# Optimization experiments

Measured on AMD Instinct MI355X. Metric: run time of the kernel, lower is better.

Reference implementation:

```python
import jax, jax.numpy as jnp
import numpy as np

M0, M1 = 16, 8          # scalar / vector multiplicities (16x0e + 8x1o)
NB = 16                  # number_of_basis
RMAX = 8.0               # max_radius
N_NODES, N_EDGES = 10000, 160000
WNUM = M0*M0 + M0*M1 + M1*M1 + M1*M0  # 576, tp weight_numel


def sus(t):
    """e3nn soft_unit_step: exp(-1/t) for t>0 else 0."""
    safe = jnp.where(t > 0, t, 1.0)
    return jnp.where(t > 0, jnp.exp(-1.0 / safe), 0.0)


def setup_inputs():
    key = jax.random.key(0)
    ks = jax.random.split(key, 12)
    D = M0 + 3 * M1  # 40
    x = jax.random.normal(ks[0], (N_NODES, D), jnp.float32)
    edge_index = jax.random.randint(ks[1], (2, N_EDGES), 0, N_NODES, jnp.int32)
    edge_attr = jax.random.normal(ks[2], (N_EDGES, 4), jnp.float32)  # sh lmax=1
    node_attr = jnp.ones((N_NODES, 1), jnp.float32)
    batch = jnp.zeros((N_NODES,), jnp.int32)
    amf = jax.random.uniform(ks[3], (N_EDGES, 1), jnp.float32) * RMAX  # edge lengths
    Wq0 = jax.random.normal(ks[4], (M0, M0), jnp.float32)
    Wq1 = jax.random.normal(ks[5], (M1, M1), jnp.float32)
    Wk1 = jax.random.normal(ks[6], (NB, 16), jnp.float32)
    Wk2 = jax.random.normal(ks[7], (16, WNUM), jnp.float32)
    Wv1 = jax.random.normal(ks[8], (NB, 16), jnp.float32)
    Wv2 = jax.random.normal(ks[9], (16, WNUM), jnp.float32)
    Wd0 = jax.random.normal(ks[10], (M0, M0), jnp.float32)
    Wd1 = jax.random.normal(ks[11], (M1, M1), jnp.float32)
    return dict(x=x, edge_index=edge_index, edge_attr=edge_attr, node_attr=node_attr,
                batch=batch, additional_message_features=amf,
                Wq0=Wq0, Wq1=Wq1, Wk1=Wk1, Wk2=Wk2, Wv1=Wv1, Wv2=Wv2, Wd0=Wd0, Wd1=Wd1)


def reference(x, edge_index, edge_attr, node_attr, batch, additional_message_features,
              Wq0, Wq1, Wk1, Wk2, Wv1, Wv2, Wd0, Wd1):
    n = x.shape[0]
    src, dst = edge_index[0], edge_index[1]
    d = additional_message_features.reshape(-1)  # [E]

    # soft_one_hot_linspace(basis='smooth_finite', cutoff=True) * sqrt(NB)
    centers = jnp.linspace(0.0, RMAX, NB + 2)[1:-1]
    step = RMAX / (NB + 1)
    diff = (d[:, None] - centers) / step
    emb = (1.14136 * np.exp(2.0)) * sus(diff + 1.0) * sus(1.0 - diff) * np.sqrt(NB)  # [E,NB]
    cutoff = sus(10.0 * (1.0 - d / RMAX))  # [E]

    # split irreps: scalars [*,M0], vectors [*,M1,3]
    x0 = x[:, :M0]
    x1 = x[:, M0:].reshape(n, M1, 3)

    # q = Linear(input_irreps -> hidden_irreps): per-irrep linear, 1/sqrt(fan_in)
    q0 = (x0 @ Wq0) / np.sqrt(M0)
    q1 = jnp.einsum('nui,uw->nwi', x1, Wq1) / np.sqrt(M1)

    # radial MLPs producing per-edge tensor-product weights
    def radial(W1, W2):
        h = jax.nn.silu((emb @ W1) / np.sqrt(NB))
        return (h @ W2) / np.sqrt(16.0)  # [E, WNUM]
    wk = radial(Wk1, Wk2)
    wv = radial(Wv1, Wv2)

    xs0, xs1 = x0[src], x1[src]           # gather by edge source
    sh0, sh1 = edge_attr[:, 0], edge_attr[:, 1:4]
    dot11 = jnp.einsum('eui,ei->eu', xs1, sh1) / np.sqrt(3.0)  # 1o x 1o -> 0e CG

    def fctp(w):
        # FullyConnectedTensorProduct(input, sh, out) with per-edge weights.
        s1 = M0 * M0
        s2 = s1 + M0 * M1
        s3 = s2 + M1 * M1
        w1 = w[:, :s1].reshape(-1, M0, M0)   # 0e x 0e -> 0e
        w2 = w[:, s1:s2].reshape(-1, M0, M1) # 0e x 1o -> 1o
        w3 = w[:, s2:s3].reshape(-1, M1, M1) # 1o x 0e -> 1o
        w4 = w[:, s3:].reshape(-1, M1, M0)   # 1o x 1o -> 0e
        norm = 1.0 / np.sqrt(M0 + M1)        # path fan-in normalization
        o0 = (jnp.einsum('euw,eu->ew', w1, xs0 * sh0[:, None]) +
              jnp.einsum('euw,eu->ew', w4, dot11)) * norm            # [E,M0]
        o1 = (jnp.einsum('euw,eu,ei->ewi', w2, xs0, sh1) +
              jnp.einsum('euw,eui->ewi', w3, xs1 * sh0[:, None, None])) * norm  # [E,M1,3]
        return o0, o1

    k0, k1 = fctp(wk)
    v0, v1 = fctp(wv)

    # dot: FullyConnectedTensorProduct(hidden, hidden, '0e') with shared weights
    score = (jnp.einsum('eu,ev,uv->e', q0[dst], k0, Wd0) +
             jnp.einsum('eui,evi,uv->e', q1[dst], k1, Wd1) / np.sqrt(3.0)) / np.sqrt(M0*M0 + M1*M1)

    expv = cutoff * jnp.exp(score)                                   # [E]
    z = jax.ops.segment_sum(expv, dst, num_segments=n)               # [N]
    z = jnp.where(z == 0, 1.0, z)
    alpha = expv / z[dst]
    we = jnp.sqrt(jax.nn.relu(alpha))                                # alpha.relu().sqrt()
    v = jnp.concatenate([v0, v1.reshape(-1, 3 * M1)], axis=1)        # [E,40]
    return jax.ops.segment_sum(we[:, None] * v, dst, num_segments=n) # [N,40]
```

## Files before the change

kernel.cpp:

```cpp
#include <hip/hip_runtime.h>
#include <hip/hip_bf16.h>

#define E_CNT 160000
#define N_CNT 10000

#define INV_STEP   2.125f
#define EMB_C      33.734292f
#define INVS320    0.05590170f
#define INVS8      0.35355339f
#define INV_SQRT3  0.57735027f
#define KSCALE     0.051031036f

#define OFF_FLAG   0
#define OFF_EAF    400016
#define OFF_AMFF   1040016
#define OFF_WK1F   1200656
#define OFF_WV1F   1200912
#define OFF_P      1219600
#define OFF_EXPV   1619600
#define OFF_VBUF   1779600
#define OFF_DEG    8179600
#define OFF_Z      8179600
#define OFF_DEG2   8189600
#define OFF_START  8199600
#define OFF_START2 8209601
#define OFF_CURS   8219602
#define OFF_CURS2  8229602
#define OFF_DPOS   8239602
#define OFF_ELIST2 8399602
#define OFF_G      8559632


static __device__ __forceinline__ float bf2f(__hip_bfloat16 b) { return __bfloat162float(b); }
static __device__ __forceinline__ float sanitize(float v) {
    return fminf(fmaxf(v, -1e30f), 1e30f);
}
static __device__ __forceinline__ unsigned short f2bf(float f) {
    unsigned x = __float_as_uint(f);
    unsigned r = (x + 0x7fffu + ((x >> 16) & 1u)) >> 16;
    return (unsigned short)r;
}
static __device__ __forceinline__ float bflo(unsigned u) { return __uint_as_float(u << 16); }
static __device__ __forceinline__ float bfhi(unsigned u) { return __uint_as_float(u & 0xffff0000u); }
static __device__ __forceinline__ float2 bfp(unsigned u) {
    float2 r; r.x = bflo(u); r.y = bfhi(u); return r;
}

static __device__ __forceinline__ float4 load4(const void* p, int i4, int f32)
{
    if (f32) return ((const float4*)p)[i4];
    uint2 u = ((const uint2*)p)[i4];
    float4 r;
    r.x = bflo(u.x); r.y = bfhi(u.x);
    r.z = bflo(u.y); r.w = bfhi(u.y);
    return r;
}

static __device__ __forceinline__ void ld8(const float* p, float (&r)[8])
{
    float4 a = ((const float4*)p)[0];
    float4 b = ((const float4*)p)[1];
    r[0] = a.x; r[1] = a.y; r[2] = a.z; r[3] = a.w;
    r[4] = b.x; r[5] = b.y; r[6] = b.z; r[7] = b.w;
}
static __device__ __forceinline__ void ld8(const __hip_bfloat16* p, float (&r)[8])
{
    uint4 u = *(const uint4*)p;
    r[0] = bflo(u.x); r[1] = bfhi(u.x); r[2] = bflo(u.y); r[3] = bfhi(u.y);
    r[4] = bflo(u.z); r[5] = bfhi(u.z); r[6] = bflo(u.w); r[7] = bfhi(u.w);
}

__global__ __launch_bounds__(256) void init_kernel(
    const unsigned short* __restrict__ xb, float* __restrict__ ws)
{
    const int idx = blockIdx.x * 256 + threadIdx.x;
    if (idx < 20000) ((int*)(ws + OFF_DEG))[idx] = 0;
    if (blockIdx.x == 0 && threadIdx.x < 64) {
        const int lane = threadIdx.x;
        unsigned e0 = (unsigned)((xb[2 * lane] >> 7) & 0xFF);
        unsigned e1 = (unsigned)((xb[128 + 2 * lane] >> 7) & 0xFF);
        int c = (e0 >= 141 ? 1 : 0) + (e1 >= 141 ? 1 : 0);
#pragma unroll
        for (int off = 1; off < 64; off <<= 1) c += __shfl_xor(c, off);
        if (lane == 0) *(int*)ws = (c >= 8) ? 1 : 0;
    }
}

static __device__ __forceinline__ void do_prep(
    const void* __restrict__ ea, const void* __restrict__ amf,
    const void* __restrict__ Wk1, const void* __restrict__ Wv1,
    const int* __restrict__ ei, float* __restrict__ ws, int i, int f32)
{
    if (i < 160000) ((float4*)(ws + OFF_EAF))[i] = load4(ea, i, f32);
    if (i < 40000) {
        ((float4*)(ws + OFF_AMFF))[i] = load4(amf, i, f32);
#pragma unroll
        for (int k = 0; k < 4; ++k) {
            atomicAdd((int*)(ws + OFF_DEG)  + ei[E_CNT + 4 * i + k], 1);
            atomicAdd((int*)(ws + OFF_DEG2) + ei[4 * i + k], 1);
        }
    }
    if (i < 64) {
        ((float4*)(ws + OFF_WK1F))[i] = load4(Wk1, i, f32);
        ((float4*)(ws + OFF_WV1F))[i] = load4(Wv1, i, f32);
    }
}

template <typename T>
static __device__ __forceinline__ void build_G(
    const T* __restrict__ x, const T* __restrict__ W2b, int n, int p, int c, float* __restrict__ ws)
{
    float xs[40];
#pragma unroll
    for (int q = 0; q < 5; ++q) ld8(x + n * 40 + q * 8, *(float(*)[8])(xs + q * 8));
    const T* W2 = W2b + c * 576;

    float out[96];
#pragma unroll
    for (int k = 0; k < 96; ++k) out[k] = 0.f;

#pragma unroll
    for (int u = 0; u < 16; ++u) {
        float r0[8], r1[8];
        ld8(W2 + u * 16, r0);
        ld8(W2 + u * 16 + 8, r1);
        const float xv = xs[u];
#pragma unroll
        for (int w = 0; w < 8; ++w) {
            out[w]     = fmaf(r0[w], xv, out[w]);
            out[8 + w] = fmaf(r1[w], xv, out[8 + w]);
        }
    }
#pragma unroll
    for (int u = 0; u < 16; ++u) {
        float r[8];
        ld8(W2 + 256 + u * 8, r);
        const float xv = xs[u];
#pragma unroll
        for (int w = 0; w < 8; ++w) out[16 + w] = fmaf(r[w], xv, out[16 + w]);
    }
#pragma unroll
    for (int u = 0; u < 8; ++u) {
        float r[8];
        ld8(W2 + 384 + u * 8, r);
        const float a0 = xs[16 + u * 3 + 0];
        const float a1 = xs[16 + u * 3 + 1];
        const float a2 = xs[16 + u * 3 + 2];
#pragma unroll
        for (int w = 0; w < 8; ++w) {
            out[24 + w * 3 + 0] = fmaf(r[w], a0, out[24 + w * 3 + 0]);
            out[24 + w * 3 + 1] = fmaf(r[w], a1, out[24 + w * 3 + 1]);
            out[24 + w * 3 + 2] = fmaf(r[w], a2, out[24 + w * 3 + 2]);
        }
    }
#pragma unroll
    for (int u = 0; u < 8; ++u) {
        float r0[8], r1[8];
        ld8(W2 + 448 + u * 16, r0);
        ld8(W2 + 448 + u * 16 + 8, r1);
        const float a0 = xs[16 + u * 3 + 0];
        const float a1 = xs[16 + u * 3 + 1];
        const float a2 = xs[16 + u * 3 + 2];
#pragma unroll
        for (int w = 0; w < 8; ++w) {
            out[48 + w * 3 + 0] = fmaf(r0[w], a0, out[48 + w * 3 + 0]);
            out[48 + w * 3 + 1] = fmaf(r0[w], a1, out[48 + w * 3 + 1]);
            out[48 + w * 3 + 2] = fmaf(r0[w], a2, out[48 + w * 3 + 2]);
            out[48 + (8 + w) * 3 + 0] = fmaf(r1[w], a0, out[48 + (8 + w) * 3 + 0]);
            out[48 + (8 + w) * 3 + 1] = fmaf(r1[w], a1, out[48 + (8 + w) * 3 + 1]);
            out[48 + (8 + w) * 3 + 2] = fmaf(r1[w], a2, out[48 + (8 + w) * 3 + 2]);
        }
    }
#pragma unroll
    for (int k = 0; k < 48; ++k) out[48 + k] *= INV_SQRT3;

    uint4 ov[12];
    unsigned* ou = (unsigned*)ov;
#pragma unroll
    for (int k = 0; k < 48; ++k)
        ou[k] = (unsigned)f2bf(out[2 * k]) | ((unsigned)f2bf(out[2 * k + 1]) << 16);
    uint4* gb = (uint4*)(ws + OFF_G) + (size_t)(p * 16 + c) * 120000 + n;
#pragma unroll
    for (int q = 0; q < 12; ++q) gb[q * 10000] = ov[q];
}

template <typename T>
static __device__ __forceinline__ void build_P(
    const T* __restrict__ x, const T* __restrict__ Wq0, const T* __restrict__ Wq1,
    const T* __restrict__ Wd0, const T* __restrict__ Wd1, int n, float* __restrict__ ws)
{
    float xs[40];
#pragma unroll
    for (int q = 0; q < 5; ++q) ld8(x + n * 40 + q * 8, *(float(*)[8])(xs + q * 8));

    float q0[16];
#pragma unroll
    for (int w = 0; w < 16; ++w) q0[w] = 0.f;
#pragma unroll
    for (int u = 0; u < 16; ++u) {
        float r0[8], r1[8];
        ld8(Wq0 + u * 16, r0);
        ld8(Wq0 + u * 16 + 8, r1);
        const float xv = xs[u];
#pragma unroll
        for (int w = 0; w < 8; ++w) {
            q0[w]     = fmaf(r0[w], xv, q0[w]);
            q0[8 + w] = fmaf(r1[w], xv, q0[8 + w]);
        }
    }
#pragma unroll
    for (int w = 0; w < 16; ++w) q0[w] *= 0.25f;

    float p0[16];
#pragma unroll
    for (int v = 0; v < 16; ++v) p0[v] = 0.f;
#pragma unroll
    for (int w = 0; w < 16; ++w) {
        float r0[8], r1[8];
        ld8(Wd0 + w * 16, r0);
        ld8(Wd0 + w * 16 + 8, r1);
        const float qv = q0[w];
#pragma unroll
        for (int v = 0; v < 8; ++v) {
            p0[v]     = fmaf(r0[v], qv, p0[v]);
            p0[8 + v] = fmaf(r1[v], qv, p0[8 + v]);
        }
    }
    float* pn = ws + OFF_P + n * 40;
#pragma unroll
    for (int v = 0; v < 16; ++v) pn[v] = sanitize(p0[v] * INVS320);

    float q1[24];
#pragma unroll
    for (int k = 0; k < 24; ++k) q1[k] = 0.f;
#pragma unroll
    for (int u = 0; u < 8; ++u) {
        float r[8];
        ld8(Wq1 + u * 8, r);
        const float a0 = xs[16 + u * 3 + 0];
        const float a1 = xs[16 + u * 3 + 1];
        const float a2 = xs[16 + u * 3 + 2];
#pragma unroll
        for (int w = 0; w < 8; ++w) {
            q1[w * 3 + 0] = fmaf(r[w], a0, q1[w * 3 + 0]);
            q1[w * 3 + 1] = fmaf(r[w], a1, q1[w * 3 + 1]);
            q1[w * 3 + 2] = fmaf(r[w], a2, q1[w * 3 + 2]);
        }
    }
#pragma unroll
    for (int k = 0; k < 24; ++k) q1[k] *= INVS8;

    float p1[24];
#pragma unroll
    for (int k = 0; k < 24; ++k) p1[k] = 0.f;
#pragma unroll
    for (int w = 0; w < 8; ++w) {
        float r[8];
        ld8(Wd1 + w * 8, r);
        const float b0 = q1[w * 3 + 0];
        const float b1 = q1[w * 3 + 1];
        const float b2 = q1[w * 3 + 2];
#pragma unroll
        for (int v = 0; v < 8; ++v) {
            p1[v * 3 + 0] = fmaf(r[v], b0, p1[v * 3 + 0]);
            p1[v * 3 + 1] = fmaf(r[v], b1, p1[v * 3 + 1]);
            p1[v * 3 + 2] = fmaf(r[v], b2, p1[v * 3 + 2]);
        }
    }
    const float sc = INVS320 * INV_SQRT3;
#pragma unroll
    for (int k = 0; k < 24; ++k) pn[16 + k] = sanitize(p1[k] * sc);
}

__global__ __launch_bounds__(256) void gp_kernel(
    const void* __restrict__ x,
    const void* __restrict__ Wq0, const void* __restrict__ Wq1,
    const void* __restrict__ Wk2, const void* __restrict__ Wv2,
    const void* __restrict__ Wd0, const void* __restrict__ Wd1,
    const void* __restrict__ ea, const void* __restrict__ amf,
    const void* __restrict__ Wk1, const void* __restrict__ Wv1,
    const int* __restrict__ ei,
    float* __restrict__ ws)
{
    const int f32 = *(const int*)ws;
    const int tid = threadIdx.x;
    const int blk = blockIdx.x;
    if (blk < 625) {
        do_prep(ea, amf, Wk1, Wv1, ei, ws, blk * 256 + tid, f32);
        return;
    }
    if (blk < 1875) {
        const int t = (blk - 625) * 256 + tid;
        const int p   = t / 160000;
        const int rem = t - p * 160000;
        const int c   = rem / 10000;
        const int n   = rem - c * 10000;
        const void* W2b = p ? Wv2 : Wk2;
        if (f32) build_G((const float*)x, (const float*)W2b, n, p, c, ws);
        else     build_G((const __hip_bfloat16*)x, (const __hip_bfloat16*)W2b, n, p, c, ws);
        return;
    }
    {
        const int n = (blk - 1875) * 256 + tid;
        if (n >= N_CNT) return;
        if (f32) build_P((const float*)x, (const float*)Wq0, (const float*)Wq1,
                         (const float*)Wd0, (const float*)Wd1, n, ws);
        else     build_P((const __hip_bfloat16*)x, (const __hip_bfloat16*)Wq0,
                         (const __hip_bfloat16*)Wq1, (const __hip_bfloat16*)Wd0,
                         (const __hip_bfloat16*)Wd1, n, ws);
    }
}

__global__ __launch_bounds__(512) void scan_kernel(float* __restrict__ ws)
{
    __shared__ int ssum[512];
    const int t    = threadIdx.x;
    const int half = t >> 8;
    const int lt   = t & 255;
    int* deg   = (int*)(ws + (half ? OFF_DEG2   : OFF_DEG));
    int* start = (int*)(ws + (half ? OFF_START2 : OFF_START));
    int* curs  = (int*)(ws + (half ? OFF_CURS2  : OFF_CURS));
    const int base = lt * 40;
    int s = 0;
    for (int k = 0; k < 40; ++k) {
        int idx = base + k;
        if (idx < N_CNT) s += deg[idx];
    }
    ssum[t] = s;
    __syncthreads();
    for (int off = 1; off < 256; off <<= 1) {
        int v = (lt >= off) ? ssum[t - off] : 0;
        __syncthreads();
        ssum[t] += v;
        __syncthreads();
    }
    int run = ssum[t] - s;
    for (int k = 0; k < 40; ++k) {
        int idx = base + k;
        if (idx < N_CNT) {
            start[idx] = run;
            curs[idx]  = run;
            run += deg[idx];
        }
    }
    if (lt == 255) start[N_CNT] = E_CNT;
    __syncthreads();
    for (int k = t; k < N_CNT; k += 512) ws[OFF_Z + k] = 0.f;
}

__global__ __launch_bounds__(256) void fill_kernel(const int* __restrict__ ei, float* __restrict__ ws)
{
    const int e = blockIdx.x * 256 + threadIdx.x;
    int pd = atomicAdd((int*)(ws + OFF_CURS)  + ei[E_CNT + e], 1);
    int ps = atomicAdd((int*)(ws + OFF_CURS2) + ei[e], 1);
    ((int*)(ws + OFF_ELIST2))[ps] = e;
    ((int*)(ws + OFF_DPOS))[ps]   = pd;
}

static __device__ __forceinline__ void load48p(unsigned (&ub)[48], const uint4* __restrict__ p0)
{
#pragma unroll
    for (int q = 0; q < 12; ++q) {
        uint4 v = p0[(size_t)q * 10000];
        ub[4 * q + 0] = v.x; ub[4 * q + 1] = v.y;
        ub[4 * q + 2] = v.z; ub[4 * q + 3] = v.w;
    }
}

static __device__ __forceinline__ void accum48(const unsigned (&ub)[48], float hc, float sh0,
    float s1x, float s1y, float s1z,
    float (&o0)[16], float (&o1)[24], float (&t2a)[8])
{
    const float hs = hc * sh0;
#define GVAL(k) (((k) & 1) ? bfhi(ub[(k) >> 1]) : bflo(ub[(k) >> 1]))
#pragma unroll
    for (int w = 0; w < 16; ++w) o0[w] = fmaf(hs, GVAL(w), o0[w]);
#pragma unroll
    for (int w = 0; w < 8; ++w) t2a[w] = fmaf(hc, GVAL(16 + w), t2a[w]);
#pragma unroll
    for (int k = 0; k < 24; ++k) o1[k] = fmaf(hs, GVAL(24 + k), o1[k]);
#pragma unroll
    for (int w = 0; w < 16; ++w) {
        float g = GVAL(48 + w * 3 + 0) * s1x;
        g = fmaf(GVAL(48 + w * 3 + 1), s1y, g);
        g = fmaf(GVAL(48 + w * 3 + 2), s1z, g);
        o0[w] = fmaf(hc, g, o0[w]);
    }
#undef GVAL
}

__global__ __launch_bounds__(128) void edge_kernel(
    const int* __restrict__ ei, float* __restrict__ ws)
{
    const int tid  = threadIdx.x;
    const int pass = tid >> 6;
    const int lane = tid & 63;
    const int b  = blockIdx.x;
    const int lb = (b < 2496) ? ((b & 7) * 312 + (b >> 3)) : b;
    const int sidx = lb * 64 + lane;
    const int e    = ((const int*)(ws + OFF_ELIST2))[sidx];
    const int dpos = ((const int*)(ws + OFF_DPOS))[sidx];
    const int src  = ei[e];
    const int dst  = ei[E_CNT + e];

    const uint4* gb = (const uint4*)(ws + OFF_G) + (size_t)pass * 1920000 + src;
    unsigned A[48], B[48];
    load48p(A, gb);
    load48p(B, gb + 120000);

    const float d   = ws[OFF_AMFF + e];
    const float dsv = d * INV_STEP;
    const int i1 = (int)ceilf(dsv) - 1;
    const int i0 = i1 - 1;
    float e0 = 0.f, e1 = 0.f;
    {
        float t1 = dsv - (float)i0;
        float t2 = (float)(i0 + 2) - dsv;
        if (i0 >= 0 && i0 <= 15 && t2 > 0.f)
            e0 = EMB_C * expf(-1.f / t1 - 1.f / t2);
        float u1 = dsv - (float)i1;
        float u2 = (float)(i1 + 2) - dsv;
        if (i1 >= 0 && i1 <= 15 && u1 > 0.f)
            e1 = EMB_C * expf(-1.f / u1 - 1.f / u2);
    }
    const int r0i = (i0 < 0 ? 0 : (i0 > 15 ? 15 : i0)) << 4;
    const int r1i = (i1 < 0 ? 0 : (i1 > 15 ? 15 : i1)) << 4;

    const float* W1 = ws + (pass ? OFF_WV1F : OFF_WK1F);
    float h[16];
#pragma unroll
    for (int j = 0; j < 16; ++j) {
        float s = fmaf(e1, W1[r1i + j], e0 * W1[r0i + j]);
        s *= 0.25f;
        h[j] = s / (1.f + expf(-s));
    }

    const float4 eav = ((const float4*)(ws + OFF_EAF))[e];
    const float sh0 = eav.x, s1x = eav.y, s1y = eav.z, s1z = eav.w;

    float o0[16], o1[24], t2a[8];
#pragma unroll
    for (int i = 0; i < 16; ++i) o0[i] = 0.f;
#pragma unroll
    for (int i = 0; i < 24; ++i) o1[i] = 0.f;
#pragma unroll
    for (int i = 0; i < 8; ++i) t2a[i] = 0.f;

#pragma unroll
    for (int c = 0; c < 16; c += 2) {
        accum48(A, h[c], sh0, s1x, s1y, s1z, o0, o1, t2a);
        if (c + 2 < 16) load48p(A, gb + (size_t)(c + 2) * 120000);
        accum48(B, h[c + 1], sh0, s1x, s1y, s1z, o0, o1, t2a);
        if (c + 3 < 16) load48p(B, gb + (size_t)(c + 3) * 120000);
    }

#pragma unroll
    for (int w = 0; w < 8; ++w) {
        o1[w * 3 + 0] = fmaf(t2a[w], s1x, o1[w * 3 + 0]);
        o1[w * 3 + 1] = fmaf(t2a[w], s1y, o1[w * 3 + 1]);
        o1[w * 3 + 2] = fmaf(t2a[w], s1z, o1[w * 3 + 2]);
    }

    if (pass == 0) {
        const float* pd = ws + OFF_P + dst * 40;
        float sc = 0.f;
#pragma unroll
        for (int j = 0; j < 16; ++j) sc = fmaf(o0[j], pd[j], sc);
#pragma unroll
        for (int j = 0; j < 24; ++j) sc = fmaf(o1[j], pd[16 + j], sc);
        sc = fminf(fmaxf(sc * KSCALE, -60.f), 60.f);
        float ct = 10.f * (1.f - d * 0.125f);
        float cutoff = (ct > 0.f) ? expf(-1.f / ct) : 0.f;
        float ev = fmaxf(cutoff * expf(sc), 0.f);
        ws[OFF_EXPV + dpos] = ev;
        atomicAdd(ws + OFF_Z + dst, ev);
    } else {
        float vo[40];
#pragma unroll
        for (int j = 0; j < 16; ++j) vo[j] = sanitize(o0[j] * KSCALE);
#pragma unroll
        for (int j = 0; j < 24; ++j) vo[16 + j] = sanitize(o1[j] * KSCALE);
        uint4 pk[5];
        unsigned* pu = (unsigned*)pk;
#pragma unroll
        for (int k = 0; k < 20; ++k)
            pu[k] = (unsigned)f2bf(vo[2 * k]) | ((unsigned)f2bf(vo[2 * k + 1]) << 16);
        uint4* vr = (uint4*)((unsigned short*)(ws + OFF_VBUF) + (size_t)dpos * 40);
#pragma unroll
        for (int q = 0; q < 5; ++q) vr[q] = pk[q];
    }
}

__global__ __launch_bounds__(256) void gather_kernel(
    const float* __restrict__ ws, void* __restrict__ out)
{
    const int i = blockIdx.x * 256 + threadIdx.x;
    if (i >= N_CNT * 10) return;
    const int n = i / 10;
    const int q = i - n * 10;
    const int* start = (const int*)(ws + OFF_START);
    const float* expv = ws + OFF_EXPV;
    const unsigned* Vb = (const unsigned*)(ws + OFF_VBUF);
    const int s = start[n], t = start[n + 1];

    float zz = ws[OFF_Z + n];
    const float rz = (zz > 0.f) ? 1.f / zz : 1.f;

    float ax = 0.f, ay = 0.f, az = 0.f, aw = 0.f;
    for (int j = s; j < t; ++j) {
        const float we = sqrtf(fmaxf(expv[j] * rz, 0.f));
        uint2 u = *(const uint2*)(Vb + (size_t)j * 20 + 2 * q);
        float2 v0 = bfp(u.x), v1 = bfp(u.y);
        ax = fmaf(we, v0.x, ax); ay = fmaf(we, v0.y, ay);
        az = fmaf(we, v1.x, az); aw = fmaf(we, v1.y, aw);
    }
    ax = sanitize(ax); ay = sanitize(ay); az = sanitize(az); aw = sanitize(aw);
    const int f32 = *(const int*)ws;
    if (f32) {
        float4 o; o.x = ax; o.y = ay; o.z = az; o.w = aw;
        ((float4*)out)[(size_t)n * 10 + q] = o;
    } else {
        uint2 o;
        o.x = (unsigned)f2bf(ax) | ((unsigned)f2bf(ay) << 16);
        o.y = (unsigned)f2bf(az) | ((unsigned)f2bf(aw) << 16);
        ((uint2*)out)[(size_t)n * 10 + q] = o;
    }
}

extern "C" void kernel_launch(void* const* d_in, const int* in_sizes, int n_in,
                              void* d_out, int out_size, void* d_ws, size_t ws_size,
                              hipStream_t stream)
{
    (void)in_sizes; (void)n_in; (void)out_size; (void)ws_size;
    const void* x   = d_in[0];
    const int*  ei  = (const int*)d_in[1];
    const void* ea  = d_in[2];
    const void* amf = d_in[5];
    const void* Wq0 = d_in[6];
    const void* Wq1 = d_in[7];
    const void* Wk1 = d_in[8];
    const void* Wk2 = d_in[9];
    const void* Wv1 = d_in[10];
    const void* Wv2 = d_in[11];
    const void* Wd0 = d_in[12];
    const void* Wd1 = d_in[13];

    float* ws = (float*)d_ws;

    init_kernel<<<79, 256, 0, stream>>>((const unsigned short*)x, ws);
    gp_kernel<<<1915, 256, 0, stream>>>(x, Wq0, Wq1, Wk2, Wv2, Wd0, Wd1,
                                        ea, amf, Wk1, Wv1, (const int*)ei, ws);
    scan_kernel<<<1, 512, 0, stream>>>(ws);
    fill_kernel<<<625, 256, 0, stream>>>(ei, ws);
    edge_kernel<<<2500, 128, 0, stream>>>(ei, ws);
    gather_kernel<<<(N_CNT * 10 + 255) / 256, 256, 0, stream>>>(ws, d_out);
}
```

Before: 265.7 us.

## Interleave G channel pairs per node and accumulate with bf16 dot2 instructions

Stores the precomputed G tables so each node's pair of adjacent channels sits in one contiguous 384-byte row, with lo/hi output halves split across the two channel threads via lane shuffles. The edge kernel now gathers contiguous uint4 runs instead of 12 strided loads, and replaces scalar bf16 unpack plus fma with v_dot2_f32_bf16, using a hi/lo bf16 split of the float coefficients to keep accuracy. This targets both gather locality and the ALU cost of unpacking, at the price of twice as many dot instructions and a changed workspace layout.

```diff
diff --git a/kernel.cpp b/kernel.cpp
--- a/kernel.cpp
+++ b/kernel.cpp
@@ -46,6 +46,24 @@
     float2 r; r.x = bflo(u); r.y = bfhi(u); return r;
 }
 
+static __device__ __forceinline__ float dot2bf(unsigned a, unsigned b, float c)
+{
+    float d;
+    asm("v_dot2_f32_bf16 %0, %1, %2, %3" : "=v"(d) : "v"(a), "v"(b), "v"(c));
+    return d;
+}
+static __device__ __forceinline__ unsigned cvtpk2(float lo, float hi)
+{
+    unsigned r;
+    asm("v_cvt_pk_bf16_f32 %0, %1, %2" : "=v"(r) : "v"(lo), "v"(hi));
+    return r;
+}
+static __device__ __forceinline__ void splitpk(float a0, float a1, unsigned& ph, unsigned& pl)
+{
+    ph = cvtpk2(a0, a1);
+    pl = cvtpk2(a0 - bflo(ph), a1 - bfhi(ph));
+}
+
 static __device__ __forceinline__ float4 load4(const void* p, int i4, int f32)
 {
     if (f32) return ((const float4*)p)[i4];
@@ -108,7 +126,8 @@
 
 template <typename T>
 static __device__ __forceinline__ void build_G(
-    const T* __restrict__ x, const T* __restrict__ W2b, int n, int p, int c, float* __restrict__ ws)
+    const T* __restrict__ x, const T* __restrict__ W2b, int n, int p, int c, int u,
+    float* __restrict__ ws)
 {
     float xs[40];
 #pragma unroll
@@ -120,11 +139,11 @@
     for (int k = 0; k < 96; ++k) out[k] = 0.f;
 
 #pragma unroll
-    for (int u = 0; u < 16; ++u) {
+    for (int uu = 0; uu < 16; ++uu) {
         float r0[8], r1[8];
-        ld8(W2 + u * 16, r0);
-        ld8(W2 + u * 16 + 8, r1);
-        const float xv = xs[u];
+        ld8(W2 + uu * 16, r0);
+        ld8(W2 + uu * 16 + 8, r1);
+        const float xv = xs[uu];
 #pragma unroll
         for (int w = 0; w < 8; ++w) {
             out[w]     = fmaf(r0[w], xv, out[w]);
@@ -132,20 +151,20 @@
         }
     }
 #pragma unroll
-    for (int u = 0; u < 16; ++u) {
+    for (int uu = 0; uu < 16; ++uu) {
         float r[8];
-        ld8(W2 + 256 + u * 8, r);
-        const float xv = xs[u];
+        ld8(W2 + 256 + uu * 8, r);
+        const float xv = xs[uu];
 #pragma unroll
         for (int w = 0; w < 8; ++w) out[16 + w] = fmaf(r[w], xv, out[16 + w]);
     }
 #pragma unroll
-    for (int u = 0; u < 8; ++u) {
+    for (int uu = 0; uu < 8; ++uu) {
         float r[8];
-        ld8(W2 + 384 + u * 8, r);
-        const float a0 = xs[16 + u * 3 + 0];
-        const float a1 = xs[16 + u * 3 + 1];
-        const float a2 = xs[16 + u * 3 + 2];
+        ld8(W2 + 384 + uu * 8, r);
+        const float a0 = xs[16 + uu * 3 + 0];
+        const float a1 = xs[16 + uu * 3 + 1];
+        const float a2 = xs[16 + uu * 3 + 2];
 #pragma unroll
         for (int w = 0; w < 8; ++w) {
             out[24 + w * 3 + 0] = fmaf(r[w], a0, out[24 + w * 3 + 0]);
@@ -154,13 +173,13 @@
         }
     }
 #pragma unroll
-    for (int u = 0; u < 8; ++u) {
+    for (int uu = 0; uu < 8; ++uu) {
         float r0[8], r1[8];
-        ld8(W2 + 448 + u * 16, r0);
-        ld8(W2 + 448 + u * 16 + 8, r1);
-        const float a0 = xs[16 + u * 3 + 0];
-        const float a1 = xs[16 + u * 3 + 1];
-        const float a2 = xs[16 + u * 3 + 2];
+        ld8(W2 + 448 + uu * 16, r0);
+        ld8(W2 + 448 + uu * 16 + 8, r1);
+        const float a0 = xs[16 + uu * 3 + 0];
+        const float a1 = xs[16 + uu * 3 + 1];
+        const float a2 = xs[16 + uu * 3 + 2];
 #pragma unroll
         for (int w = 0; w < 8; ++w) {
             out[48 + w * 3 + 0] = fmaf(r0[w], a0, out[48 + w * 3 + 0]);
@@ -177,11 +196,18 @@
     uint4 ov[12];
     unsigned* ou = (unsigned*)ov;
 #pragma unroll
-    for (int k = 0; k < 48; ++k)
-        ou[k] = (unsigned)f2bf(out[2 * k]) | ((unsigned)f2bf(out[2 * k + 1]) << 16);
-    uint4* gb = (uint4*)(ws + OFF_G) + (size_t)(p * 16 + c) * 120000 + n;
-#pragma unroll
-    for (int q = 0; q < 12; ++q) gb[q * 10000] = ov[q];
+    for (int kk = 0; kk < 48; ++kk) {
+        float oa = __shfl_xor(out[kk], 1);
+        float ob = __shfl_xor(out[48 + kk], 1);
+        float lov = u ? ob : out[kk];
+        float hiv = u ? out[48 + kk] : oa;
+        ou[kk] = (unsigned)f2bf(lov) | ((unsigned)f2bf(hiv) << 16);
+    }
+    const int jj = (c >> 1) & 7;
+    uint4* gb = (uint4*)(ws + OFF_G)
+              + ((size_t)(p * 8 + jj) * 10000 + n) * 24 + u * 12;
+#pragma unroll
+    for (int q = 0; q < 12; ++q) gb[q] = ov[q];
 }
 
 template <typename T>
@@ -290,14 +316,17 @@
         return;
     }
     if (blk < 1875) {
-        const int t = (blk - 625) * 256 + tid;
-        const int p   = t / 160000;
-        const int rem = t - p * 160000;
-        const int c   = rem / 10000;
-        const int n   = rem - c * 10000;
+        const int t  = (blk - 625) * 256 + tid;
+        const int j2 = t / 20000;
+        const int r  = t - j2 * 20000;
+        const int n  = r >> 1;
+        const int u  = r & 1;
+        const int p  = j2 >> 3;
+        const int jj = j2 & 7;
+        const int c  = jj * 2 + u;
         const void* W2b = p ? Wv2 : Wk2;
-        if (f32) build_G((const float*)x, (const float*)W2b, n, p, c, ws);
-        else     build_G((const __hip_bfloat16*)x, (const __hip_bfloat16*)W2b, n, p, c, ws);
+        if (f32) build_G((const float*)x, (const float*)W2b, n, p, c, u, ws);
+        else     build_G((const __hip_bfloat16*)x, (const __hip_bfloat16*)W2b, n, p, c, u, ws);
         return;
     }
     {
@@ -357,36 +386,48 @@
     ((int*)(ws + OFF_DPOS))[ps]   = pd;
 }
 
-static __device__ __forceinline__ void load48p(unsigned (&ub)[48], const uint4* __restrict__ p0)
+static __device__ __forceinline__ void load12c(unsigned (&ub)[48], const uint4* __restrict__ p0)
 {
 #pragma unroll
     for (int q = 0; q < 12; ++q) {
-        uint4 v = p0[(size_t)q * 10000];
+        uint4 v = p0[q];
         ub[4 * q + 0] = v.x; ub[4 * q + 1] = v.y;
         ub[4 * q + 2] = v.z; ub[4 * q + 3] = v.w;
     }
 }
 
-static __device__ __forceinline__ void accum48(const unsigned (&ub)[48], float hc, float sh0,
-    float s1x, float s1y, float s1z,
+static __device__ __forceinline__ void accum_lo(const unsigned (&ub)[48],
+    float h0, float h1, float sh0,
     float (&o0)[16], float (&o1)[24], float (&t2a)[8])
 {
-    const float hs = hc * sh0;
-#define GVAL(k) (((k) & 1) ? bfhi(ub[(k) >> 1]) : bflo(ub[(k) >> 1]))
-#pragma unroll
-    for (int w = 0; w < 16; ++w) o0[w] = fmaf(hs, GVAL(w), o0[w]);
-#pragma unroll
-    for (int w = 0; w < 8; ++w) t2a[w] = fmaf(hc, GVAL(16 + w), t2a[w]);
-#pragma unroll
-    for (int k = 0; k < 24; ++k) o1[k] = fmaf(hs, GVAL(24 + k), o1[k]);
+    unsigned hsH, hsL, hcH, hcL;
+    splitpk(h0 * sh0, h1 * sh0, hsH, hsL);
+    splitpk(h0, h1, hcH, hcL);
+#pragma unroll
+    for (int w = 0; w < 16; ++w)
+        o0[w] = dot2bf(ub[w], hsL, dot2bf(ub[w], hsH, o0[w]));
+#pragma unroll
+    for (int w = 0; w < 8; ++w)
+        t2a[w] = dot2bf(ub[16 + w], hcL, dot2bf(ub[16 + w], hcH, t2a[w]));
+#pragma unroll
+    for (int k = 0; k < 24; ++k)
+        o1[k] = dot2bf(ub[24 + k], hsL, dot2bf(ub[24 + k], hsH, o1[k]));
+}
+static __device__ __forceinline__ void accum_hi(const unsigned (&ub)[48],
+    float h0, float h1, float s1x, float s1y, float s1z, float (&o0)[16])
+{
+    unsigned hxH, hxL, hyH, hyL, hzH, hzL;
+    splitpk(h0 * s1x, h1 * s1x, hxH, hxL);
+    splitpk(h0 * s1y, h1 * s1y, hyH, hyL);
+    splitpk(h0 * s1z, h1 * s1z, hzH, hzL);
 #pragma unroll
     for (int w = 0; w < 16; ++w) {
-        float g = GVAL(48 + w * 3 + 0) * s1x;
-        g = fmaf(GVAL(48 + w * 3 + 1), s1y, g);
-        g = fmaf(GVAL(48 + w * 3 + 2), s1z, g);
-        o0[w] = fmaf(hc, g, o0[w]);
-    }
-#undef GVAL
+        float acc = o0[w];
+        acc = dot2bf(ub[3 * w + 0], hxL, dot2bf(ub[3 * w + 0], hxH, acc));
+        acc = dot2bf(ub[3 * w + 1], hyL, dot2bf(ub[3 * w + 1], hyH, acc));
+        acc = dot2bf(ub[3 * w + 2], hzL, dot2bf(ub[3 * w + 2], hzH, acc));
+        o0[w] = acc;
+    }
 }
 
 __global__ __launch_bounds__(128) void edge_kernel(
@@ -403,10 +444,10 @@
     const int src  = ei[e];
     const int dst  = ei[E_CNT + e];
 
-    const uint4* gb = (const uint4*)(ws + OFF_G) + (size_t)pass * 1920000 + src;
+    const uint4* gb = (const uint4*)(ws + OFF_G) + ((size_t)pass * 80000 + src) * 24;
     unsigned A[48], B[48];
-    load48p(A, gb);
-    load48p(B, gb + 120000);
+    load12c(A, gb);
+    load12c(B, gb + 12);
 
     const float d   = ws[OFF_AMFF + e];
     const float dsv = d * INV_STEP;
@@ -447,11 +488,12 @@
     for (int i = 0; i < 8; ++i) t2a[i] = 0.f;
 
 #pragma unroll
-    for (int c = 0; c < 16; c += 2) {
-        accum48(A, h[c], sh0, s1x, s1y, s1z, o0, o1, t2a);
-        if (c + 2 < 16) load48p(A, gb + (size_t)(c + 2) * 120000);
-        accum48(B, h[c + 1], sh0, s1x, s1y, s1z, o0, o1, t2a);
-        if (c + 3 < 16) load48p(B, gb + (size_t)(c + 3) * 120000);
+    for (int s = 0; s < 16; s += 2) {
+        const int jj = s >> 1;
+        accum_lo(A, h[2 * jj], h[2 * jj + 1], sh0, o0, o1, t2a);
+        if (s + 2 < 16) load12c(A, gb + (size_t)(jj + 1) * 240000);
+        accum_hi(B, h[2 * jj], h[2 * jj + 1], s1x, s1y, s1z, o0);
+        if (s + 3 < 16) load12c(B, gb + (size_t)(jj + 1) * 240000 + 12);
     }
 
 #pragma unroll
```

Measured after the change: 293.5 us. +10.5%, slower.
